# Kernel optimization log

Measured on AMD Instinct MI355X. Metric: run time of the kernel, lower is better.

## Reference

```python
import jax, jax.numpy as jnp
import numpy as np

B, L, D_MODEL = 1, 1024, 768
H = 12            # num_heads == num_key_value_heads
FDIM = 16         # feature_dim
HEAD_DIM = D_MODEL // H  # 64
EPS = 1e-12
R2 = np.sqrt(2.0)
RD = np.sqrt(float(FDIM))        # sqrt(16) = 4
RRD = np.sqrt(RD)                # sqrt(4) = 2


def setup_inputs() -> dict:
    key = jax.random.key(0)
    ks = jax.random.split(key, 5)
    s = 1.0 / np.sqrt(D_MODEL)
    return {
        "hidden_states": jax.random.normal(ks[0], (B, L, D_MODEL), dtype=jnp.float32),
        "Wq": jax.random.normal(ks[1], (D_MODEL, H * FDIM), dtype=jnp.float32) * s,
        "Wk": jax.random.normal(ks[2], (D_MODEL, H * FDIM), dtype=jnp.float32) * s,
        "Wv": jax.random.normal(ks[3], (D_MODEL, D_MODEL), dtype=jnp.float32) * s,
        "Wo": jax.random.normal(ks[4], (D_MODEL, D_MODEL), dtype=jnp.float32) * s,
    }


def taylor_exp_feature_map(x):
    # x: (b, h, l, FDIM) -> (b, h, l, 1 + FDIM + FDIM^2)
    x2 = (x[..., :, None] * x[..., None, :]).reshape(*x.shape[:-1], FDIM * FDIM) / R2
    ones = jnp.ones((*x.shape[:-1], 1), dtype=x.dtype)
    return jnp.concatenate([ones, x / RRD, x2 / RD], axis=-1)


def reference(hidden_states, Wq, Wk, Wv, Wo):
    b, l, _ = hidden_states.shape
    q = (hidden_states @ Wq).reshape(b, l, H, FDIM).transpose(0, 2, 1, 3)
    k = (hidden_states @ Wk).reshape(b, l, H, FDIM).transpose(0, 2, 1, 3)
    v = (hidden_states @ Wv).reshape(b, l, H, HEAD_DIM).transpose(0, 2, 1, 3)
    q = taylor_exp_feature_map(q)  # (b,h,l,Dexp)
    k = taylor_exp_feature_map(k)  # (b,h,l,Dexp)
    # causal linear attention: y_t = q_t . cumsum_t(k_s v_s^T) / (q_t . cumsum_t(k_s) + eps)
    kv = k[..., :, None] * v[..., None, :]          # (b,h,l,Dexp,hd)
    kv_cum = jnp.cumsum(kv, axis=2)                  # (b,h,l,Dexp,hd)
    num = jnp.einsum('bhln,bhlnd->bhld', q, kv_cum)  # (b,h,l,hd)
    k_cum = jnp.cumsum(k, axis=2)                    # (b,h,l,Dexp)
    den = jnp.einsum('bhln,bhln->bhl', q, k_cum)[..., None] + EPS
    y = num / den                                    # (b,h,l,hd)
    y = y.transpose(0, 2, 1, 3).reshape(b, l, H * HEAD_DIM)
    return y @ Wo
```

## Files before the change

kernel.cpp:

```cpp
#include <hip/hip_runtime.h>

#define C2 0.17677669529663687f

typedef __attribute__((ext_vector_type(8))) short short8;
typedef __attribute__((ext_vector_type(8))) unsigned short ushort8;
typedef __attribute__((ext_vector_type(4))) float f32x4;

__device__ __forceinline__ unsigned short f2bf(float x) {
    union { float f; unsigned u; } v; v.f = x;
    unsigned r = v.u + 0x7fffu + ((v.u >> 16) & 1u);
    return (unsigned short)(r >> 16);
}
__device__ __forceinline__ float bf2f(unsigned short u) {
    union { unsigned u; float f; } v; v.u = ((unsigned)u) << 16;
    return v.f;
}

__device__ __forceinline__ void gemm_inblk_splitk(
    const float* __restrict__ A, const float* __restrict__ W,
    float* __restrict__ out, int row0, int n0, int outcol0, int ldw, int outld)
{
    __shared__ unsigned short Al[2][2][64][40];
    __shared__ unsigned short Bl[2][2][64][40];
    __shared__ float red[64][65];
    const int tid = threadIdx.x;
    const int g = tid >> 8;
    const int t = tid & 255;
    const int lane = t & 63, wave4 = t >> 6;
    const int wm = wave4 & 1, wn = wave4 >> 1;
    const int quad = lane >> 4, lr = lane & 15;
    const int k0base = g * 384;

    f32x4 acc[2][2] = {{{0.f,0.f,0.f,0.f},{0.f,0.f,0.f,0.f}},
                       {{0.f,0.f,0.f,0.f},{0.f,0.f,0.f,0.f}}};

    float4 ra[2], rb[2];
    #pragma unroll
    for (int l = 0; l < 2; ++l) {
        int idx = t + l * 256;
        ra[l] = *(const float4*)&A[(size_t)(row0 + (idx >> 3)) * 768 + k0base + (idx & 7) * 4];
        rb[l] = *(const float4*)&W[(size_t)(k0base + (idx >> 4)) * ldw + n0 + (idx & 15) * 4];
    }
    #pragma unroll
    for (int l = 0; l < 2; ++l) {
        int idx = t + l * 256;
        *(ushort4*)&Al[g][0][idx >> 3][(idx & 7) * 4] =
            make_ushort4(f2bf(ra[l].x), f2bf(ra[l].y), f2bf(ra[l].z), f2bf(ra[l].w));
        int kr = idx >> 4, nq = (idx & 15) * 4;
        int col = (((kr >> 3) ^ ((idx & 15) >> 2)) << 3) | (kr & 7);
        Bl[g][0][nq + 0][col] = f2bf(rb[l].x);
        Bl[g][0][nq + 1][col] = f2bf(rb[l].y);
        Bl[g][0][nq + 2][col] = f2bf(rb[l].z);
        Bl[g][0][nq + 3][col] = f2bf(rb[l].w);
    }
    __syncthreads();

    const int ITER = 12;
    #pragma unroll
    for (int i = 0; i < ITER; ++i) {
        const int cur = i & 1, nxt = cur ^ 1;
        float4 na[2], nb[2];
        if (i + 1 < ITER) {
            int kn = k0base + (i + 1) * 32;
            #pragma unroll
            for (int l = 0; l < 2; ++l) {
                int idx = t + l * 256;
                na[l] = *(const float4*)&A[(size_t)(row0 + (idx >> 3)) * 768 + kn + (idx & 7) * 4];
                nb[l] = *(const float4*)&W[(size_t)(kn + (idx >> 4)) * ldw + n0 + (idx & 15) * 4];
            }
        }
        short8 af[2], bfr[2];
        #pragma unroll
        for (int mi = 0; mi < 2; ++mi)
            af[mi] = *(const short8*)&Al[g][cur][wm * 32 + mi * 16 + lr][quad << 3];
        #pragma unroll
        for (int ni = 0; ni < 2; ++ni) {
            int csw = quad ^ ((wn * 2 + ni) & 3);
            bfr[ni] = *(const short8*)&Bl[g][cur][wn * 32 + ni * 16 + lr][csw << 3];
        }
        #pragma unroll
        for (int mi = 0; mi < 2; ++mi)
            #pragma unroll
            for (int ni = 0; ni < 2; ++ni)
                acc[mi][ni] = __builtin_amdgcn_mfma_f32_16x16x32_bf16(af[mi], bfr[ni], acc[mi][ni], 0, 0, 0);
        if (i + 1 < ITER) {
            #pragma unroll
            for (int l = 0; l < 2; ++l) {
                int idx = t + l * 256;
                *(ushort4*)&Al[g][nxt][idx >> 3][(idx & 7) * 4] =
                    make_ushort4(f2bf(na[l].x), f2bf(na[l].y), f2bf(na[l].z), f2bf(na[l].w));
                int kr = idx >> 4, nq = (idx & 15) * 4;
                int col = (((kr >> 3) ^ ((idx & 15) >> 2)) << 3) | (kr & 7);
                Bl[g][nxt][nq + 0][col] = f2bf(nb[l].x);
                Bl[g][nxt][nq + 1][col] = f2bf(nb[l].y);
                Bl[g][nxt][nq + 2][col] = f2bf(nb[l].z);
                Bl[g][nxt][nq + 3][col] = f2bf(nb[l].w);
            }
        }
        __syncthreads();
    }
    if (g == 1) {
        #pragma unroll
        for (int mi = 0; mi < 2; ++mi)
            #pragma unroll
            for (int ni = 0; ni < 2; ++ni)
                #pragma unroll
                for (int r = 0; r < 4; ++r)
                    red[wm * 32 + mi * 16 + quad * 4 + r][wn * 32 + ni * 16 + lr] = acc[mi][ni][r];
    }
    __syncthreads();
    if (g == 0) {
        #pragma unroll
        for (int mi = 0; mi < 2; ++mi)
            #pragma unroll
            for (int ni = 0; ni < 2; ++ni)
                #pragma unroll
                for (int r = 0; r < 4; ++r) {
                    int rr = wm * 32 + mi * 16 + quad * 4 + r;
                    int cc = wn * 32 + ni * 16 + lr;
                    out[(size_t)(row0 + rr) * outld + outcol0 + cc] = acc[mi][ni][r] + red[rr][cc];
                }
    }
}

__global__ __launch_bounds__(512) void gemm_qkv_mfma(
    const float* __restrict__ H, const float* __restrict__ Wq,
    const float* __restrict__ Wk, const float* __restrict__ Wv,
    float* __restrict__ out)
{
    const int nt = blockIdx.x, mt = blockIdx.y;
    const float* W; int ldw, n0;
    if (nt < 3)      { W = Wq; ldw = 192; n0 = nt * 64; }
    else if (nt < 6) { W = Wk; ldw = 192; n0 = (nt - 3) * 64; }
    else             { W = Wv; ldw = 768; n0 = (nt - 6) * 64; }
    gemm_inblk_splitk(H, W, out, mt * 64, n0, nt * 64, ldw, 1152);
}

__global__ __launch_bounds__(512) void gemm_wo_mfma(
    const float* __restrict__ Y, const float* __restrict__ Wo, float* __restrict__ out)
{
    const int nt = blockIdx.x, mt = blockIdx.y;
    gemm_inblk_splitk(Y, Wo, out, mt * 64, nt * 64, nt * 64, 768, 768);
}

__global__ __launch_bounds__(512) void chunk_state_k(
    const float* __restrict__ qkv, unsigned short* __restrict__ St, float* __restrict__ zb)
{
    const int c = blockIdx.x, h = blockIdx.y;
    __shared__ float Kc[64][17];
    __shared__ unsigned short Pk[320][72];
    __shared__ unsigned short Vt[80][72];
    const int tid = threadIdx.x;
    const int lane = tid & 63, wave = tid >> 6;
    const int quad = lane >> 4, lr = lane & 15;

    if (tid < 256) {
        int s = tid >> 2, f4 = (tid & 3) * 4;
        float4 kv = *(const float4*)&qkv[(size_t)(c * 64 + s) * 1152 + 192 + h * 16 + f4];
        Kc[s][f4 + 0] = kv.x; Kc[s][f4 + 1] = kv.y; Kc[s][f4 + 2] = kv.z; Kc[s][f4 + 3] = kv.w;
    }
    #pragma unroll
    for (int l = 0; l < 2; ++l) {
        int idx = tid + l * 512;
        int s = idx >> 4, d4 = (idx & 15) * 4;
        float4 vv = *(const float4*)&qkv[(size_t)(c * 64 + s) * 1152 + 384 + h * 64 + d4];
        Vt[d4 + 0][s] = f2bf(vv.x);
        Vt[d4 + 1][s] = f2bf(vv.y);
        Vt[d4 + 2][s] = f2bf(vv.z);
        Vt[d4 + 3][s] = f2bf(vv.w);
    }
    for (int idx = tid; idx < 16 * 72; idx += 512) {
        int rr = 64 + idx / 72, ss = idx % 72;
        Vt[rr][ss] = (rr == 64 && ss < 64) ? (unsigned short)0x3F80 : (unsigned short)0;
    }
    __syncthreads();
    for (int idx = tid; idx < 2880; idx += 512) {
        int n = idx / 9, s8 = (idx % 9) * 8;
        short8 v8;
        #pragma unroll
        for (int tt = 0; tt < 8; ++tt) {
            int s = s8 + tt;
            float ph = 0.f;
            if (s < 64 && n < 273) {
                if (n == 0) ph = 1.f;
                else if (n < 17) ph = Kc[s][n - 1] * 0.5f;
                else { int m = n - 17; ph = Kc[s][m >> 4] * Kc[s][m & 15] * C2; }
            }
            v8[tt] = (short)f2bf(ph);
        }
        *(short8*)&Pk[n][s8] = v8;
    }
    __syncthreads();

    f32x4 acc[5][3];
    #pragma unroll
    for (int mt = 0; mt < 5; ++mt)
        #pragma unroll
        for (int nt = 0; nt < 3; ++nt) acc[mt][nt] = (f32x4){0.f, 0.f, 0.f, 0.f};
    #pragma unroll
    for (int ks = 0; ks < 2; ++ks) {
        short8 af[5], bfr[3];
        #pragma unroll
        for (int mt = 0; mt < 5; ++mt)
            af[mt] = *(const short8*)&Vt[mt * 16 + lr][ks * 32 + quad * 8];
        #pragma unroll
        for (int nt = 0; nt < 3; ++nt)
            if (wave + 8 * nt < 20)
                bfr[nt] = *(const short8*)&Pk[(wave + 8 * nt) * 16 + lr][ks * 32 + quad * 8];
        #pragma unroll
        for (int mt = 0; mt < 5; ++mt)
            #pragma unroll
            for (int nt = 0; nt < 3; ++nt)
                if (wave + 8 * nt < 20)
                    acc[mt][nt] = __builtin_amdgcn_mfma_f32_16x16x32_bf16(af[mt], bfr[nt], acc[mt][nt], 0, 0, 0);
    }
    unsigned short* Sbt = St + (size_t)(h * 16 + c) * 18432;
    float* zp = zb + (h * 16 + c) * 273;
    #pragma unroll
    for (int nt = 0; nt < 3; ++nt) {
        int tile = wave + 8 * nt;
        if (tile < 20) {
            int n = tile * 16 + lr;
            if (n < 288) {
                #pragma unroll
                for (int mt = 0; mt < 4; ++mt)
                    #pragma unroll
                    for (int r = 0; r < 4; ++r)
                        Sbt[(mt * 16 + quad * 4 + r) * 288 + n] =
                            (n < 273) ? f2bf(acc[mt][nt][r]) : (unsigned short)0;
                if (quad == 0 && n < 273) zp[n] = acc[4][nt][0];
            }
        }
    }
}

__global__ __launch_bounds__(256) void scan_state_k(unsigned short* __restrict__ St, float* __restrict__ z)
{
    const int NV = 12 * 64 * 36;
    int gid = blockIdx.x * 256 + threadIdx.x;
    if (gid < NV) {
        int hh = gid / (64 * 36), rem = gid % (64 * 36);
        int d = rem / 36, nb = rem % 36;
        unsigned short* p = St + (size_t)hh * 16 * 18432 + d * 288 + nb * 8;
        ushort8 v[16];
        #pragma unroll
        for (int cc = 0; cc < 16; ++cc) v[cc] = *(const ushort8*)(p + (size_t)cc * 18432);
        float run[8] = {0.f,0.f,0.f,0.f,0.f,0.f,0.f,0.f};
        #pragma unroll
        for (int cc = 0; cc < 16; ++cc) {
            ushort8 w;
            #pragma unroll
            for (int j = 0; j < 8; ++j) {
                w[j] = f2bf(run[j]);
                run[j] += bf2f(v[cc][j]);
            }
            *(ushort8*)(p + (size_t)cc * 18432) = w;
        }
    } else if (gid < NV + 12 * 273) {
        int e2 = gid - NV, hh = e2 / 273, n = e2 % 273;
        float* p = z + hh * 16 * 273 + n;
        float v[16];
        #pragma unroll
        for (int cc = 0; cc < 16; ++cc) v[cc] = p[cc * 273];
        float run = 0.f;
        #pragma unroll
        for (int cc = 0; cc < 16; ++cc) { p[cc * 273] = run; run += v[cc]; }
    }
}

__global__ __launch_bounds__(512) void chunk_out_k(
    const float* __restrict__ qkv, const unsigned short* __restrict__ St, const float* __restrict__ z,
    float* __restrict__ y)
{
    const int c = blockIdx.x, h = blockIdx.y;
    __shared__ float Qc[64][17];
    __shared__ unsigned short Aq[64][40];
    __shared__ unsigned short Kb[64][40];
    __shared__ unsigned short Pq[64][360];
    __shared__ unsigned short Vt[64][72];
    __shared__ float zl[288];
    __shared__ float dpart[12][64];
    const int tid = threadIdx.x;
    const int lane = tid & 63, wave = tid >> 6;
    const int quad = lane >> 4, lr = lane & 15;
    const int wm = wave & 1, wn = wave >> 1;

    const unsigned short* Sgt = St + (size_t)(h * 16 + c) * 18432;
    short8 sfr[9];
    #pragma unroll
    for (int ks = 0; ks < 9; ++ks)
        sfr[ks] = *(const short8*)&Sgt[(wn * 16 + lr) * 288 + ks * 32 + quad * 8];

    if (tid < 256) {
        int s = tid >> 2, f4 = (tid & 3) * 4;
        const float* base = &qkv[(size_t)(c * 64 + s) * 1152 + h * 16];
        float4 qv = *(const float4*)&base[f4];
        float4 kv = *(const float4*)&base[192 + f4];
        Qc[s][f4 + 0] = qv.x; Qc[s][f4 + 1] = qv.y; Qc[s][f4 + 2] = qv.z; Qc[s][f4 + 3] = qv.w;
        *(ushort4*)&Aq[s][f4] = make_ushort4(f2bf(qv.x), f2bf(qv.y), f2bf(qv.z), f2bf(qv.w));
        *(ushort4*)&Kb[s][f4] = make_ushort4(f2bf(kv.x), f2bf(kv.y), f2bf(kv.z), f2bf(kv.w));
        *(ushort4*)&Aq[s][16 + (tid & 3) * 4] = make_ushort4(0, 0, 0, 0);
        *(ushort4*)&Kb[s][16 + (tid & 3) * 4] = make_ushort4(0, 0, 0, 0);
    }
    #pragma unroll
    for (int l = 0; l < 2; ++l) {
        int idx = tid + l * 512;
        int ss = idx >> 4, d4 = (idx & 15) * 4;
        float4 vv = *(const float4*)&qkv[(size_t)(c * 64 + ss) * 1152 + 384 + h * 64 + d4];
        Vt[d4 + 0][ss] = f2bf(vv.x);
        Vt[d4 + 1][ss] = f2bf(vv.y);
        Vt[d4 + 2][ss] = f2bf(vv.z);
        Vt[d4 + 3][ss] = f2bf(vv.w);
    }
    const float* zg = z + (h * 16 + c) * 273;
    for (int idx = tid; idx < 288; idx += 512) zl[idx] = (idx < 273) ? zg[idx] : 0.f;
    __syncthreads();

    f32x4 accS[2] = {{0.f,0.f,0.f,0.f},{0.f,0.f,0.f,0.f}};
    {
        short8 bfr = *(const short8*)&Kb[wn * 16 + lr][quad * 8];
        #pragma unroll
        for (int mi = 0; mi < 2; ++mi) {
            short8 af = *(const short8*)&Aq[wm * 32 + mi * 16 + lr][quad * 8];
            accS[mi] = __builtin_amdgcn_mfma_f32_16x16x32_bf16(af, bfr, accS[mi], 0, 0, 0);
        }
    }

    {
        int i = lane;
        float qr[16];
        #pragma unroll
        for (int f = 0; f < 16; ++f) qr[f] = Qc[i][f];
        float dp = 0.f;
        int n0 = wave * 36;
        for (int n = n0; n < n0 + 36; ++n) {
            float ph;
            if (n == 0) ph = 1.f;
            else if (n < 17) ph = qr[n - 1] * 0.5f;
            else if (n < 273) { int m = n - 17; ph = qr[m >> 4] * qr[m & 15] * C2; }
            else ph = 0.f;
            Pq[i][n] = f2bf(ph);
            dp += ph * zl[n];
        }
        dpart[wave][i] = dp;
    }

    #pragma unroll
    for (int mi = 0; mi < 2; ++mi) {
        float rs[4];
        #pragma unroll
        for (int r = 0; r < 4; ++r) {
            int i = wm * 32 + mi * 16 + quad * 4 + r;
            int j = wn * 16 + lr;
            float u = accS[mi][r];
            float sc = (j <= i) ? (1.f + 0.25f * u + u * u * (1.f / 32.f)) : 0.f;
            rs[r] = sc;
            Pq[i][288 + j] = f2bf(sc);
        }
        #pragma unroll
        for (int r = 0; r < 4; ++r) {
            float v = rs[r];
            v += __shfl_xor(v, 1);
            v += __shfl_xor(v, 2);
            v += __shfl_xor(v, 4);
            v += __shfl_xor(v, 8);
            if (lr == 0) dpart[8 + wn][wm * 32 + mi * 16 + quad * 4 + r] = v;
        }
    }
    __syncthreads();

    f32x4 acc[2] = {{0.f,0.f,0.f,0.f},{0.f,0.f,0.f,0.f}};
    #pragma unroll
    for (int ks = 0; ks < 11; ++ks) {
        short8 bfr = (ks < 9)
            ? sfr[ks]
            : *(const short8*)&Vt[wn * 16 + lr][(ks - 9) * 32 + quad * 8];
        #pragma unroll
        for (int mi = 0; mi < 2; ++mi) {
            short8 af = *(const short8*)&Pq[wm * 32 + mi * 16 + lr][ks * 32 + quad * 8];
            acc[mi] = __builtin_amdgcn_mfma_f32_16x16x32_bf16(af, bfr, acc[mi], 0, 0, 0);
        }
    }

    #pragma unroll
    for (int mi = 0; mi < 2; ++mi)
        #pragma unroll
        for (int r = 0; r < 4; ++r) {
            int i = wm * 32 + mi * 16 + quad * 4 + r;
            float den = 1e-12f;
            #pragma unroll
            for (int w = 0; w < 12; ++w) den += dpart[w][i];
            float rden = 1.f / den;
            y[(size_t)(c * 64 + i) * 768 + h * 64 + wn * 16 + lr] = acc[mi][r] * rden;
        }
}

extern "C" void kernel_launch(void* const* d_in, const int* in_sizes, int n_in,
                              void* d_out, int out_size, void* d_ws, size_t ws_size,
                              hipStream_t stream) {
    const float* hs = (const float*)d_in[0];
    const float* Wq = (const float*)d_in[1];
    const float* Wk = (const float*)d_in[2];
    const float* Wv = (const float*)d_in[3];
    const float* Wo = (const float*)d_in[4];
    float* out = (float*)d_out;
    float* ws  = (float*)d_ws;

    float* qkv = ws;
    float* yb  = ws + 1179648;
    unsigned short* St = (unsigned short*)(ws + 1966080);
    float* zb  = ws + 5320704;

    gemm_qkv_mfma<<<dim3(18, 16), 512, 0, stream>>>(hs, Wq, Wk, Wv, qkv);
    chunk_state_k<<<dim3(16, 12), 512, 0, stream>>>(qkv, St, zb);
    scan_state_k <<<121, 256, 0, stream>>>(St, zb);
    chunk_out_k  <<<dim3(16, 12), 512, 0, stream>>>(qkv, St, zb, yb);
    gemm_wo_mfma <<<dim3(12, 16), 512, 0, stream>>>(yb, Wo, out);
}
```

Before: 120.5 us.

## Pre-convert inputs and weights to bf16 and pass bf16 intermediates between stages

Adds a conversion kernel that turns hidden states and all four weight matrices into bf16 once per call. The GEMMs then load bf16 tiles directly instead of loading fp32 and converting in the inner loop. The QKV GEMM also writes a bf16 copy of its output, and V is written only in bf16. The attention kernels read bf16 Q/K/V, and the attention output y is stored in bf16 for the Wo GEMM. This halves global traffic and removes conversion work from the GEMM loops, at the cost of an extra launch and a full pass over the weights each call.

```diff
diff --git a/kernel.cpp b/kernel.cpp
--- a/kernel.cpp
+++ b/kernel.cpp
@@ -16,12 +16,36 @@
     return v.f;
 }
 
-__device__ __forceinline__ void gemm_inblk_splitk(
-    const float* __restrict__ A, const float* __restrict__ W,
-    float* __restrict__ out, int row0, int n0, int outcol0, int ldw, int outld)
-{
-    __shared__ unsigned short Al[2][2][64][40];
-    __shared__ unsigned short Bl[2][2][64][40];
+__global__ __launch_bounds__(512) void cvt_prep(
+    const float* __restrict__ hs, const float* __restrict__ Wq, const float* __restrict__ Wk,
+    const float* __restrict__ Wv, const float* __restrict__ Wo,
+    unsigned short* __restrict__ Hh, unsigned short* __restrict__ Wqh,
+    unsigned short* __restrict__ Wkh, unsigned short* __restrict__ Wvh,
+    unsigned short* __restrict__ Woh)
+{
+    int e8 = (blockIdx.x * 512 + threadIdx.x) * 8;
+    const float* src; unsigned short* dst; int off;
+    if      (e8 < 786432)  { src = hs; dst = Hh;  off = e8; }
+    else if (e8 < 933888)  { src = Wq; dst = Wqh; off = e8 - 786432; }
+    else if (e8 < 1081344) { src = Wk; dst = Wkh; off = e8 - 933888; }
+    else if (e8 < 1671168) { src = Wv; dst = Wvh; off = e8 - 1081344; }
+    else                   { src = Wo; dst = Woh; off = e8 - 1671168; }
+    float4 a = *(const float4*)&src[off];
+    float4 b = *(const float4*)&src[off + 4];
+    ushort8 o;
+    o[0] = f2bf(a.x); o[1] = f2bf(a.y); o[2] = f2bf(a.z); o[3] = f2bf(a.w);
+    o[4] = f2bf(b.x); o[5] = f2bf(b.y); o[6] = f2bf(b.z); o[7] = f2bf(b.w);
+    *(ushort8*)&dst[off] = o;
+}
+
+__device__ __forceinline__ void gemm_inblk_splitk_h(
+    const unsigned short* __restrict__ A,
+    const unsigned short* __restrict__ W,
+    float* __restrict__ out, unsigned short* __restrict__ outh,
+    int row0, int n0, int outcol0, int ldw, int outld, bool write_f32)
+{
+    __shared__ __align__(16) unsigned short Al[2][2][64][40];
+    __shared__ __align__(16) unsigned short Bl[2][2][64][40];
     __shared__ float red[64][65];
     const int tid = threadIdx.x;
     const int g = tid >> 8;
@@ -30,28 +54,22 @@
     const int wm = wave4 & 1, wn = wave4 >> 1;
     const int quad = lane >> 4, lr = lane & 15;
     const int k0base = g * 384;
+    const int ar = t >> 2, ak8 = (t & 3) * 8;
+    const int bkr = t >> 3, bn8 = (t & 7) * 8;
 
     f32x4 acc[2][2] = {{{0.f,0.f,0.f,0.f},{0.f,0.f,0.f,0.f}},
                        {{0.f,0.f,0.f,0.f},{0.f,0.f,0.f,0.f}}};
 
-    float4 ra[2], rb[2];
-    #pragma unroll
-    for (int l = 0; l < 2; ++l) {
-        int idx = t + l * 256;
-        ra[l] = *(const float4*)&A[(size_t)(row0 + (idx >> 3)) * 768 + k0base + (idx & 7) * 4];
-        rb[l] = *(const float4*)&W[(size_t)(k0base + (idx >> 4)) * ldw + n0 + (idx & 15) * 4];
-    }
-    #pragma unroll
-    for (int l = 0; l < 2; ++l) {
-        int idx = t + l * 256;
-        *(ushort4*)&Al[g][0][idx >> 3][(idx & 7) * 4] =
-            make_ushort4(f2bf(ra[l].x), f2bf(ra[l].y), f2bf(ra[l].z), f2bf(ra[l].w));
-        int kr = idx >> 4, nq = (idx & 15) * 4;
-        int col = (((kr >> 3) ^ ((idx & 15) >> 2)) << 3) | (kr & 7);
-        Bl[g][0][nq + 0][col] = f2bf(rb[l].x);
-        Bl[g][0][nq + 1][col] = f2bf(rb[l].y);
-        Bl[g][0][nq + 2][col] = f2bf(rb[l].z);
-        Bl[g][0][nq + 3][col] = f2bf(rb[l].w);
+    {
+        ushort8 ra = *(const ushort8*)&A[(size_t)(row0 + ar) * 768 + k0base + ak8];
+        ushort8 rb = *(const ushort8*)&W[(size_t)(k0base + bkr) * ldw + n0 + bn8];
+        *(ushort8*)&Al[g][0][ar][ak8] = ra;
+        #pragma unroll
+        for (int j = 0; j < 8; ++j) {
+            int n = bn8 + j;
+            int col = (((bkr >> 3) ^ (n >> 4)) << 3) | (bkr & 7);
+            Bl[g][0][n][col] = rb[j];
+        }
     }
     __syncthreads();
 
@@ -59,15 +77,11 @@
     #pragma unroll
     for (int i = 0; i < ITER; ++i) {
         const int cur = i & 1, nxt = cur ^ 1;
-        float4 na[2], nb[2];
+        ushort8 na, nb;
         if (i + 1 < ITER) {
             int kn = k0base + (i + 1) * 32;
-            #pragma unroll
-            for (int l = 0; l < 2; ++l) {
-                int idx = t + l * 256;
-                na[l] = *(const float4*)&A[(size_t)(row0 + (idx >> 3)) * 768 + kn + (idx & 7) * 4];
-                nb[l] = *(const float4*)&W[(size_t)(kn + (idx >> 4)) * ldw + n0 + (idx & 15) * 4];
-            }
+            na = *(const ushort8*)&A[(size_t)(row0 + ar) * 768 + kn + ak8];
+            nb = *(const ushort8*)&W[(size_t)(kn + bkr) * ldw + n0 + bn8];
         }
         short8 af[2], bfr[2];
         #pragma unroll
@@ -84,17 +98,12 @@
             for (int ni = 0; ni < 2; ++ni)
                 acc[mi][ni] = __builtin_amdgcn_mfma_f32_16x16x32_bf16(af[mi], bfr[ni], acc[mi][ni], 0, 0, 0);
         if (i + 1 < ITER) {
-            #pragma unroll
-            for (int l = 0; l < 2; ++l) {
-                int idx = t + l * 256;
-                *(ushort4*)&Al[g][nxt][idx >> 3][(idx & 7) * 4] =
-                    make_ushort4(f2bf(na[l].x), f2bf(na[l].y), f2bf(na[l].z), f2bf(na[l].w));
-                int kr = idx >> 4, nq = (idx & 15) * 4;
-                int col = (((kr >> 3) ^ ((idx & 15) >> 2)) << 3) | (kr & 7);
-                Bl[g][nxt][nq + 0][col] = f2bf(nb[l].x);
-                Bl[g][nxt][nq + 1][col] = f2bf(nb[l].y);
-                Bl[g][nxt][nq + 2][col] = f2bf(nb[l].z);
-                Bl[g][nxt][nq + 3][col] = f2bf(nb[l].w);
+            *(ushort8*)&Al[g][nxt][ar][ak8] = na;
+            #pragma unroll
+            for (int j = 0; j < 8; ++j) {
+                int n = bn8 + j;
+                int col = (((bkr >> 3) ^ (n >> 4)) << 3) | (bkr & 7);
+                Bl[g][nxt][n][col] = nb[j];
             }
         }
         __syncthreads();
@@ -118,33 +127,38 @@
                 for (int r = 0; r < 4; ++r) {
                     int rr = wm * 32 + mi * 16 + quad * 4 + r;
                     int cc = wn * 32 + ni * 16 + lr;
-                    out[(size_t)(row0 + rr) * outld + outcol0 + cc] = acc[mi][ni][r] + red[rr][cc];
+                    float v = acc[mi][ni][r] + red[rr][cc];
+                    if (write_f32) out[(size_t)(row0 + rr) * outld + outcol0 + cc] = v;
+                    if (outh) outh[(size_t)(row0 + rr) * outld + outcol0 + cc] = f2bf(v);
                 }
     }
 }
 
 __global__ __launch_bounds__(512) void gemm_qkv_mfma(
-    const float* __restrict__ H, const float* __restrict__ Wq,
-    const float* __restrict__ Wk, const float* __restrict__ Wv,
+    const unsigned short* __restrict__ Hh, const unsigned short* __restrict__ Wqh,
+    const unsigned short* __restrict__ Wkh, const unsigned short* __restrict__ Wvh,
+    float* __restrict__ out, unsigned short* __restrict__ outh)
+{
+    const int nt = blockIdx.x, mt = blockIdx.y;
+    const unsigned short* W; int ldw, n0;
+    if (nt < 3)      { W = Wqh; ldw = 192; n0 = nt * 64; }
+    else if (nt < 6) { W = Wkh; ldw = 192; n0 = (nt - 3) * 64; }
+    else             { W = Wvh; ldw = 768; n0 = (nt - 6) * 64; }
+    gemm_inblk_splitk_h(Hh, W, out, outh, mt * 64, n0, nt * 64, ldw, 1152, nt < 6);
+}
+
+__global__ __launch_bounds__(512) void gemm_wo_mfma(
+    const unsigned short* __restrict__ Yh, const unsigned short* __restrict__ Woh,
     float* __restrict__ out)
 {
     const int nt = blockIdx.x, mt = blockIdx.y;
-    const float* W; int ldw, n0;
-    if (nt < 3)      { W = Wq; ldw = 192; n0 = nt * 64; }
-    else if (nt < 6) { W = Wk; ldw = 192; n0 = (nt - 3) * 64; }
-    else             { W = Wv; ldw = 768; n0 = (nt - 6) * 64; }
-    gemm_inblk_splitk(H, W, out, mt * 64, n0, nt * 64, ldw, 1152);
-}
-
-__global__ __launch_bounds__(512) void gemm_wo_mfma(
-    const float* __restrict__ Y, const float* __restrict__ Wo, float* __restrict__ out)
-{
-    const int nt = blockIdx.x, mt = blockIdx.y;
-    gemm_inblk_splitk(Y, Wo, out, mt * 64, nt * 64, nt * 64, 768, 768);
+    gemm_inblk_splitk_h(Yh, Woh, out, (unsigned short*)nullptr,
+                        mt * 64, nt * 64, nt * 64, 768, 768, true);
 }
 
 __global__ __launch_bounds__(512) void chunk_state_k(
-    const float* __restrict__ qkv, unsigned short* __restrict__ St, float* __restrict__ zb)
+    const float* __restrict__ qkv, const unsigned short* __restrict__ qkvh,
+    unsigned short* __restrict__ St, float* __restrict__ zb)
 {
     const int c = blockIdx.x, h = blockIdx.y;
     __shared__ float Kc[64][17];
@@ -159,15 +173,11 @@
         float4 kv = *(const float4*)&qkv[(size_t)(c * 64 + s) * 1152 + 192 + h * 16 + f4];
         Kc[s][f4 + 0] = kv.x; Kc[s][f4 + 1] = kv.y; Kc[s][f4 + 2] = kv.z; Kc[s][f4 + 3] = kv.w;
     }
-    #pragma unroll
-    for (int l = 0; l < 2; ++l) {
-        int idx = tid + l * 512;
-        int s = idx >> 4, d4 = (idx & 15) * 4;
-        float4 vv = *(const float4*)&qkv[(size_t)(c * 64 + s) * 1152 + 384 + h * 64 + d4];
-        Vt[d4 + 0][s] = f2bf(vv.x);
-        Vt[d4 + 1][s] = f2bf(vv.y);
-        Vt[d4 + 2][s] = f2bf(vv.z);
-        Vt[d4 + 3][s] = f2bf(vv.w);
+    {
+        int s = tid >> 3, d8 = (tid & 7) * 8;
+        ushort8 vv = *(const ushort8*)&qkvh[(size_t)(c * 64 + s) * 1152 + 384 + h * 64 + d8];
+        #pragma unroll
+        for (int j = 0; j < 8; ++j) Vt[d8 + j][s] = vv[j];
     }
     for (int idx = tid; idx < 16 * 72; idx += 512) {
         int rr = 64 + idx / 72, ss = idx % 72;
@@ -269,8 +279,9 @@
 }
 
 __global__ __launch_bounds__(512) void chunk_out_k(
-    const float* __restrict__ qkv, const unsigned short* __restrict__ St, const float* __restrict__ z,
-    float* __restrict__ y)
+    const float* __restrict__ qkv, const unsigned short* __restrict__ qkvh,
+    const unsigned short* __restrict__ St, const float* __restrict__ z,
+    unsigned short* __restrict__ y)
 {
     const int c = blockIdx.x, h = blockIdx.y;
     __shared__ float Qc[64][17];
@@ -293,24 +304,20 @@
 
     if (tid < 256) {
         int s = tid >> 2, f4 = (tid & 3) * 4;
-        const float* base = &qkv[(size_t)(c * 64 + s) * 1152 + h * 16];
-        float4 qv = *(const float4*)&base[f4];
-        float4 kv = *(const float4*)&base[192 + f4];
+        float4 qv = *(const float4*)&qkv[(size_t)(c * 64 + s) * 1152 + h * 16 + f4];
         Qc[s][f4 + 0] = qv.x; Qc[s][f4 + 1] = qv.y; Qc[s][f4 + 2] = qv.z; Qc[s][f4 + 3] = qv.w;
-        *(ushort4*)&Aq[s][f4] = make_ushort4(f2bf(qv.x), f2bf(qv.y), f2bf(qv.z), f2bf(qv.w));
-        *(ushort4*)&Kb[s][f4] = make_ushort4(f2bf(kv.x), f2bf(kv.y), f2bf(kv.z), f2bf(kv.w));
+        *(ushort4*)&Aq[s][f4] =
+            *(const ushort4*)&qkvh[(size_t)(c * 64 + s) * 1152 + h * 16 + f4];
+        *(ushort4*)&Kb[s][f4] =
+            *(const ushort4*)&qkvh[(size_t)(c * 64 + s) * 1152 + 192 + h * 16 + f4];
         *(ushort4*)&Aq[s][16 + (tid & 3) * 4] = make_ushort4(0, 0, 0, 0);
         *(ushort4*)&Kb[s][16 + (tid & 3) * 4] = make_ushort4(0, 0, 0, 0);
     }
-    #pragma unroll
-    for (int l = 0; l < 2; ++l) {
-        int idx = tid + l * 512;
-        int ss = idx >> 4, d4 = (idx & 15) * 4;
-        float4 vv = *(const float4*)&qkv[(size_t)(c * 64 + ss) * 1152 + 384 + h * 64 + d4];
-        Vt[d4 + 0][ss] = f2bf(vv.x);
-        Vt[d4 + 1][ss] = f2bf(vv.y);
-        Vt[d4 + 2][ss] = f2bf(vv.z);
-        Vt[d4 + 3][ss] = f2bf(vv.w);
+    {
+        int ss = tid >> 3, d8 = (tid & 7) * 8;
+        ushort8 vv = *(const ushort8*)&qkvh[(size_t)(c * 64 + ss) * 1152 + 384 + h * 64 + d8];
+        #pragma unroll
+        for (int j = 0; j < 8; ++j) Vt[d8 + j][ss] = vv[j];
     }
     const float* zg = z + (h * 16 + c) * 273;
     for (int idx = tid; idx < 288; idx += 512) zl[idx] = (idx < 273) ? zg[idx] : 0.f;
@@ -391,7 +398,7 @@
             #pragma unroll
             for (int w = 0; w < 12; ++w) den += dpart[w][i];
             float rden = 1.f / den;
-            y[(size_t)(c * 64 + i) * 768 + h * 64 + wn * 16 + lr] = acc[mi][r] * rden;
+            y[(size_t)(c * 64 + i) * 768 + h * 64 + wn * 16 + lr] = f2bf(acc[mi][r] * rden);
         }
 }
 
@@ -406,14 +413,21 @@
     float* out = (float*)d_out;
     float* ws  = (float*)d_ws;
 
-    float* qkv = ws;
-    float* yb  = ws + 1179648;
-    unsigned short* St = (unsigned short*)(ws + 1966080);
-    float* zb  = ws + 5320704;
-
-    gemm_qkv_mfma<<<dim3(18, 16), 512, 0, stream>>>(hs, Wq, Wk, Wv, qkv);
-    chunk_state_k<<<dim3(16, 12), 512, 0, stream>>>(qkv, St, zb);
+    float*          qkv  = ws;
+    unsigned short* qkvh = (unsigned short*)(ws + 1179648);
+    unsigned short* yb   = (unsigned short*)(ws + 1769472);
+    unsigned short* St   = (unsigned short*)(ws + 2162688);
+    float*          zb   = ws + 3932160;
+    unsigned short* Hh   = (unsigned short*)(ws + 3984576);
+    unsigned short* Wqh  = (unsigned short*)(ws + 4377792);
+    unsigned short* Wkh  = (unsigned short*)(ws + 4451520);
+    unsigned short* Wvh  = (unsigned short*)(ws + 4525248);
+    unsigned short* Woh  = (unsigned short*)(ws + 4820160);
+
+    cvt_prep     <<<552, 512, 0, stream>>>(hs, Wq, Wk, Wv, Wo, Hh, Wqh, Wkh, Wvh, Woh);
+    gemm_qkv_mfma<<<dim3(18, 16), 512, 0, stream>>>(Hh, Wqh, Wkh, Wvh, qkv, qkvh);
+    chunk_state_k<<<dim3(16, 12), 512, 0, stream>>>(qkv, qkvh, St, zb);
     scan_state_k <<<121, 256, 0, stream>>>(St, zb);
-    chunk_out_k  <<<dim3(16, 12), 512, 0, stream>>>(qkv, St, zb, yb);
-    gemm_wo_mfma <<<dim3(12, 16), 512, 0, stream>>>(yb, Wo, out);
-}
+    chunk_out_k  <<<dim3(16, 12), 512, 0, stream>>>(qkv, qkvh, St, zb, yb);
+    gemm_wo_mfma <<<dim3(12, 16), 512, 0, stream>>>(yb, Woh, out);
+}
```

After: 119.0 us. No clear change (-1.3%).
